# Performance work log

Measured on AMD Instinct MI355X. Metric: run time of the kernel, lower is better.

Reference implementation:

```python
import jax, jax.numpy as jnp
import numpy as np

EPS = 1e-8  # EPS is referenced but undefined in the original source; standard small epsilon


def setup_inputs() -> dict:
    key = jax.random.key(0)
    ks = jax.random.split(key, 12)
    B, T, F = 8, 512, 512
    H, maxlen = 8, 1024
    dh = F // H
    s = 0.02
    return {
        "x": jax.random.normal(ks[0], (B, T, F), jnp.float32),
        "Wq": jax.random.normal(ks[1], (F, F), jnp.float32) * s,
        "bq": jax.random.normal(ks[2], (F,), jnp.float32) * s,
        "Wk": jax.random.normal(ks[3], (F, F), jnp.float32) * s,
        "bk": jax.random.normal(ks[4], (F,), jnp.float32) * s,
        "Wv": jax.random.normal(ks[5], (F, F), jnp.float32) * s,
        "bv": jax.random.normal(ks[6], (F,), jnp.float32) * s,
        "Wo": jax.random.normal(ks[7], (F, F), jnp.float32) * s,
        "bo": jax.random.normal(ks[8], (F,), jnp.float32) * s,
        "delta": jnp.ones((1,), jnp.float32),
        "cache_k": jax.random.normal(ks[9], (B * H, maxlen, dh), jnp.float32),
        "cache_v": jax.random.normal(ks[10], (B * H, maxlen, dh), jnp.float32),
    }


def _to_heads(y, B, T, H, dh):
    # torch.cat(torch.split(y, dh, dim=-1), dim=0): head-major (H*B, T, dh)
    return y.reshape(B, T, H, dh).transpose(2, 0, 1, 3).reshape(H * B, T, dh)


def reference(x, Wq, bq, Wk, bk, Wv, bv, Wo, bo, delta, cache_k, cache_v):
    B, T, F = x.shape
    maxlen, dh = cache_k.shape[1], cache_k.shape[2]
    H = F // dh

    q = _to_heads(x @ Wq.T + bq, B, T, H, dh)  # (HB, T, dh)
    k_new = _to_heads(x @ Wk.T + bk, B, T, H, dh)
    v_new = _to_heads(x @ Wv.T + bv, B, T, H, dh)

    # streaming cache: drop oldest T frames, append new
    k = jnp.concatenate([cache_k[:, T:], k_new], axis=1)  # (HB, maxlen, dh)
    v = jnp.concatenate([cache_v[:, T:], v_new], axis=1)

    # Gaussian relative-position mask G[i,j] = exp(-(i-j)^2 / (delta^2 + EPS))
    ind = jnp.arange(1, maxlen + 1, dtype=x.dtype)
    diff = ind[:, None] - ind[None, :]
    G = jnp.exp(-(diff ** 2) / (delta[0] ** 2 + EPS))  # (maxlen, maxlen)

    d = jnp.sqrt(jnp.asarray(F, jnp.float32)).astype(x.dtype)
    scores = jnp.einsum("btd,bsd->bts", q, k) * G[-T:][None] / d  # (HB, T, maxlen)
    attn = jax.nn.softmax(scores, axis=-1)
    out = jnp.einsum("bts,bsd->btd", attn, v)  # (HB, T, dh)

    # undo head-major split: cat(split(out, B, dim=0), dim=-1)
    out = out.reshape(H, B, T, dh).transpose(1, 2, 0, 3).reshape(B, T, F)
    return out @ Wo.T + bo
```

## Files before the change

### kernel.cpp

```cpp
#include <hip/hip_runtime.h>

typedef __bf16 bf16;
typedef __bf16 bf16x8 __attribute__((ext_vector_type(8)));
typedef __bf16 bf16x4 __attribute__((ext_vector_type(4)));
typedef float f32x4 __attribute__((ext_vector_type(4)));
typedef float f32x16 __attribute__((ext_vector_type(16)));

#define MFMA16(a, b, c) __builtin_amdgcn_mfma_f32_16x16x32_bf16((a), (b), (c), 0, 0, 0)
#define MFMA32(a, b, c) __builtin_amdgcn_mfma_f32_32x32x16_bf16((a), (b), (c), 0, 0, 0)

__device__ __forceinline__ void gload_lds16(const void* g, void* l) {
  __builtin_amdgcn_global_load_lds(
      (const __attribute__((address_space(1))) void*)g,
      (__attribute__((address_space(3))) void*)l, 16, 0, 0);
}

__global__ __launch_bounds__(256) void prep_all(
    const float* __restrict__ x, const float* __restrict__ w0, const float* __restrict__ w1,
    const float* __restrict__ w2, const float* __restrict__ w3, const float* __restrict__ delta,
    const float* __restrict__ ck, const float* __restrict__ cv,
    bf16* __restrict__ xb, bf16* __restrict__ o0, bf16* __restrict__ o1,
    bf16* __restrict__ o2, bf16* __restrict__ o3, float* __restrict__ gt,
    bf16* __restrict__ kk, bf16* __restrict__ vt) {
  const int bid = blockIdx.x;
  const int tid = threadIdx.x;
  __shared__ bf16 tl[64][65];

  if (bid < 2048) {
    const int i = (bid * 256 + tid) * 4;
    f32x4 v = *(const f32x4*)(x + i);
    bf16x4 o;
    o[0] = (bf16)v[0]; o[1] = (bf16)v[1]; o[2] = (bf16)v[2]; o[3] = (bf16)v[3];
    *(bf16x4*)(xb + i) = o;
  } else if (bid < 3072) {
    const int wb = bid - 2048;
    const int widx = wb >> 8;
    const float* s = widx == 0 ? w0 : widx == 1 ? w1 : widx == 2 ? w2 : w3;
    bf16* d = widx == 0 ? o0 : widx == 1 ? o1 : widx == 2 ? o2 : o3;
    const int i = ((wb & 255) * 256 + tid) * 4;
    f32x4 v = *(const f32x4*)(s + i);
    bf16x4 o;
    o[0] = (bf16)v[0]; o[1] = (bf16)v[1]; o[2] = (bf16)v[2]; o[3] = (bf16)v[3];
    *(bf16x4*)(d + i) = o;
  } else if (bid < 3584) {
    const int b2 = bid - 3072;
    const int hb = b2 >> 3;
    const int s0 = (b2 & 7) * 64;
#pragma unroll
    for (int it = 0; it < 16; ++it) {
      int idx = it * 256 + tid;
      int sl = idx >> 6, dd = idx & 63;
      float kval = ck[((size_t)hb * 1024 + 512 + s0 + sl) * 64 + dd];
      kk[((size_t)hb * 1024 + s0 + sl) * 64 + dd] = (bf16)kval;
      float vval = cv[((size_t)hb * 1024 + 512 + s0 + sl) * 64 + dd];
      tl[sl][dd] = (bf16)vval;
    }
    __syncthreads();
#pragma unroll
    for (int it = 0; it < 16; ++it) {
      int idx = it * 256 + tid;
      int dl = idx >> 6, sl = idx & 63;
      vt[((size_t)hb * 64 + dl) * 1024 + s0 + sl] = tl[sl][dl];
    }
  } else {
    const int i = (bid - 3584) * 256 + tid;
    if (i < 1535) {
      float dl = delta[0];
      float inv = 1.0f / (dl * dl + 1e-8f);
      float diff = (float)(i - 511);
      gt[i] = __expf(-diff * diff * inv) * 0.04419417382415922f * 1.4426950408889634f;
    }
  }
}

__global__ __launch_bounds__(256) void qkv_gemm(const bf16* __restrict__ xb,
                                                const bf16* __restrict__ wq, const bf16* __restrict__ wk,
                                                const bf16* __restrict__ wv,
                                                const float* __restrict__ bq, const float* __restrict__ bk,
                                                const float* __restrict__ bv,
                                                bf16* __restrict__ qh, bf16* __restrict__ kk,
                                                bf16* __restrict__ vt) {
  __shared__ bf16 As[128 * 32];
  __shared__ bf16 Bs[64 * 32];
  const int tid = threadIdx.x;
  const int lane = tid & 63;
  const int wave = tid >> 6;
  const int l15 = lane & 15, lg = lane >> 4;
  const int mbase = blockIdx.x * 128;
  const int nfull = blockIdx.y * 64;
  const int mid = nfull >> 9;
  const int nbase = nfull & 511;
  const bf16* W = mid == 0 ? wq : (mid == 1 ? wk : wv);
  const float* bias = mid == 0 ? bq : (mid == 1 ? bk : bv);
  f32x4 acc[2][4] = {};

  const int oB = tid * 16;
  const int rowB = oB >> 6;
  const int cbB = oB & 63;
  for (int k0 = 0; k0 < 512; k0 += 32) {
    __syncthreads();
#pragma unroll
    for (int t = 0; t < 2; ++t) {
      const int oA = (t * 256 + tid) * 16;
      gload_lds16((const char*)(xb + (size_t)(mbase + (oA >> 6)) * 512 + k0) + (oA & 63),
                  (char*)As + oA);
    }
    gload_lds16((const char*)(W + (size_t)(nbase + rowB) * 512 + k0) + cbB, (char*)Bs + oB);
    __syncthreads();
    bf16x8 af[2], bfr[4];
#pragma unroll
    for (int i = 0; i < 2; ++i)
      af[i] = *(const bf16x8*)(As + (wave * 32 + i * 16 + l15) * 32 + lg * 8);
#pragma unroll
    for (int j = 0; j < 4; ++j)
      bfr[j] = *(const bf16x8*)(Bs + (j * 16 + l15) * 32 + lg * 8);
#pragma unroll
    for (int i = 0; i < 2; ++i)
#pragma unroll
      for (int j = 0; j < 4; ++j)
        acc[i][j] = MFMA16(af[i], bfr[j], acc[i][j]);
  }

#pragma unroll
  for (int j = 0; j < 4; ++j) {
    const int nn = nbase + j * 16 + l15;
    const float bvv = bias[nn];
    const int h = nn >> 6, dd = nn & 63;
#pragma unroll
    for (int i = 0; i < 2; ++i) {
#pragma unroll
      for (int r = 0; r < 4; ++r) {
        const int mr = mbase + wave * 32 + i * 16 + lg * 4 + r;
        const float v = acc[i][j][r] + bvv;
        const int bb = mr >> 9, t = mr & 511;
        if (mid == 0) {
          qh[(((size_t)(h * 8 + bb) * 512 + t) << 6) + dd] = (bf16)v;
        } else if (mid == 1) {
          kk[(((size_t)(h * 8 + bb) * 1024 + 512 + t) << 6) + dd] = (bf16)v;
        } else {
          vt[(((size_t)(h * 8 + bb) * 64 + dd) << 10) + 512 + t] = (bf16)v;
        }
      }
    }
  }
}

__global__ __launch_bounds__(256) void out_gemm(const bf16* __restrict__ A,
                                                const bf16* __restrict__ W,
                                                const float* __restrict__ bias,
                                                float* __restrict__ out) {
  __shared__ bf16 As[64 * 32];
  __shared__ bf16 Bs[64 * 32];
  const int tid = threadIdx.x;
  const int lane = tid & 63;
  const int wave = tid >> 6;
  const int wr = wave >> 1, wc = wave & 1;
  const int l15 = lane & 15, lg = lane >> 4;
  const int mbase = blockIdx.x * 64;
  const int nbase = blockIdx.y * 64;
  f32x4 acc[2][2] = {};

  const int o = tid * 16;
  const int row = o >> 6;
  const int cb = o & 63;
  for (int k0 = 0; k0 < 512; k0 += 32) {
    __syncthreads();
    gload_lds16((const char*)(A + (size_t)(mbase + row) * 512 + k0) + cb, (char*)As + o);
    gload_lds16((const char*)(W + (size_t)(nbase + row) * 512 + k0) + cb, (char*)Bs + o);
    __syncthreads();
    bf16x8 af[2], bfr[2];
#pragma unroll
    for (int i = 0; i < 2; ++i)
      af[i] = *(const bf16x8*)(As + (wr * 32 + i * 16 + l15) * 32 + lg * 8);
#pragma unroll
    for (int j = 0; j < 2; ++j)
      bfr[j] = *(const bf16x8*)(Bs + (wc * 32 + j * 16 + l15) * 32 + lg * 8);
#pragma unroll
    for (int i = 0; i < 2; ++i)
#pragma unroll
      for (int j = 0; j < 2; ++j)
        acc[i][j] = MFMA16(af[i], bfr[j], acc[i][j]);
  }

#pragma unroll
  for (int j = 0; j < 2; ++j) {
    const int nn = nbase + wc * 32 + j * 16 + l15;
    const float bvv = bias[nn];
#pragma unroll
    for (int i = 0; i < 2; ++i) {
#pragma unroll
      for (int r = 0; r < 4; ++r) {
        const int mr = mbase + wr * 32 + i * 16 + lg * 4 + r;
        out[(size_t)mr * 512 + nn] = acc[i][j][r] + bvv;
      }
    }
  }
}

__global__ __launch_bounds__(256) void attn_k(const bf16* __restrict__ qh,
                                              const bf16* __restrict__ kk,
                                              const bf16* __restrict__ vt,
                                              const float* __restrict__ gtab,
                                              bf16* __restrict__ ao) {
  const int bid = blockIdx.x;
  const int xcd = bid & 7;
  const int g = bid >> 3;
  const int hb = xcd * 8 + (g >> 3);
  const int qp = g & 7;
  const int tid = threadIdx.x;
  const int lane = tid & 63;
  const int wave = tid >> 6;
  const int l31 = lane & 31;
  const int hi = lane >> 5;
  const int qtile = qp * 2 + (wave & 1);
  const int kvhalf = wave >> 1;
  const int qbase = qtile * 32;
  const int t = qbase + l31;

  __shared__ float gl[1536];
  __shared__ __align__(16) bf16 pbuf[4][32][40];
  __shared__ float mbuf[2][64][33];
  __shared__ float mlb[2][64][2];

  for (int i = tid; i < 1535; i += 256) gl[i] = gtab[i];

  const bf16* qrow = qh + ((size_t)hb * 512 + t) * 64 + hi * 8;
  bf16x8 qf0 = *(const bf16x8*)(qrow);
  bf16x8 qf1 = *(const bf16x8*)(qrow + 16);
  bf16x8 qf2 = *(const bf16x8*)(qrow + 32);
  bf16x8 qf3 = *(const bf16x8*)(qrow + 48);

  const bf16* kbase = kk + (size_t)hb * 1024 * 64;
  const bf16* vbase = vt + (size_t)hb * 64 * 1024;
  const bf16* krow = kbase + (size_t)l31 * 64 + hi * 8;
  const bf16* vrow = vbase + (size_t)l31 * 1024 + hi * 8;

  const int sb0 = kvhalf * 512;
  float m_r = -3.0e38f, l_r = 0.f;
  f32x16 accA = {}, accB = {};

  __syncthreads();

  bf16x8 kc0, kc1, kc2, kc3, kn0, kn1, kn2, kn3;
  {
    const bf16* kp = krow + (size_t)sb0 * 64;
    kc0 = *(const bf16x8*)(kp);
    kc1 = *(const bf16x8*)(kp + 16);
    kc2 = *(const bf16x8*)(kp + 32);
    kc3 = *(const bf16x8*)(kp + 48);
  }

#define ATTN_STEP(C0, C1, C2, C3, N0, N1, N2, N3, SB, PF)                       \
  {                                                                             \
    f32x16 c = {};                                                              \
    c = MFMA32(C0, qf0, c);                                                     \
    c = MFMA32(C1, qf1, c);                                                     \
    c = MFMA32(C2, qf2, c);                                                     \
    c = MFMA32(C3, qf3, c);                                                     \
    if (PF) {                                         \
      const bf16* kp_ = krow + (size_t)((SB) + 32) * 64;                        \
      N0 = *(const bf16x8*)(kp_);                                               \
      N1 = *(const bf16x8*)(kp_ + 16);                                          \
      N2 = *(const bf16x8*)(kp_ + 32);                                          \
      N3 = *(const bf16x8*)(kp_ + 48);                                          \
    }                                                                           \
                                                   \
    const bf16* vp_ = vrow + (SB);                                              \
    bf16x8 vf00 = *(const bf16x8*)(vp_);                                        \
    bf16x8 vf01 = *(const bf16x8*)(vp_ + 16);                                   \
    bf16x8 vf10 = *(const bf16x8*)(vp_ + 32768);                                \
    bf16x8 vf11 = *(const bf16x8*)(vp_ + 32768 + 16);                           \
     \
    const int BASE = 1023 + t - (SB)-4 * hi;                                    \
    float x[16];                                                                \
    _Pragma("unroll") for (int gq = 0; gq < 4; ++gq)                            \
        _Pragma("unroll") for (int j = 0; j < 4; ++j)                           \
            x[gq * 4 + j] = c[gq * 4 + j] * gl[BASE - 8 * gq - j];              \
    float pm = x[0];                                                            \
    _Pragma("unroll") for (int r = 1; r < 16; ++r) pm = fmaxf(pm, x[r]);        \
    pm = fmaxf(pm, __shfl_xor(pm, 32, 64));                                     \
    if (!__all(pm <= m_r + 12.0f)) {             \
      const float mn = fmaxf(m_r, pm);                                          \
      const float fac = exp2f(m_r - mn);                                        \
      m_r = mn;                                                                 \
      l_r *= fac;                                                               \
      _Pragma("unroll") for (int r = 0; r < 16; ++r) {                          \
        accA[r] *= fac;                                                         \
        accB[r] *= fac;                                                         \
      }                                                                         \
    }                                                                           \
    float ps = 0.f;                                                             \
    float e[16];                                                                \
    _Pragma("unroll") for (int r = 0; r < 16; ++r) {                            \
      e[r] = exp2f(x[r] - m_r);                                                 \
      ps += e[r];                                                               \
    }                                                                           \
                      \
    _Pragma("unroll") for (int gq = 0; gq < 4; ++gq) {                          \
      bf16x4 pw;                                                                \
      _Pragma("unroll") for (int j = 0; j < 4; ++j) pw[j] = (bf16)e[gq * 4 + j];\
      *(bf16x4*)&pbuf[wave][l31][4 * hi + 8 * gq] = pw;                         \
    }                                                                           \
    ps += __shfl_xor(ps, 32, 64);                                               \
    l_r += ps;                                                                  \
    asm volatile("s_waitcnt lgkmcnt(0)" ::: "memory");                          \
    __builtin_amdgcn_sched_barrier(0);                                          \
                  \
    bf16x8 P0 = *(const bf16x8*)&pbuf[wave][l31][8 * hi];                       \
    bf16x8 P1 = *(const bf16x8*)&pbuf[wave][l31][16 + 8 * hi];                  \
    accA = MFMA32(vf00, P0, accA);                                              \
    accA = MFMA32(vf01, P1, accA);                                              \
    accB = MFMA32(vf10, P0, accB);                                              \
    accB = MFMA32(vf11, P1, accB);                                              \
  }

  int sb = sb0;
#pragma unroll 1
  for (int it2 = 0; it2 < 8; ++it2) {
    ATTN_STEP(kc0, kc1, kc2, kc3, kn0, kn1, kn2, kn3, sb, true);
    ATTN_STEP(kn0, kn1, kn2, kn3, kc0, kc1, kc2, kc3, sb + 32, it2 < 7);
    sb += 64;
  }
#undef ATTN_STEP

  __syncthreads();
  const int slot = wave & 1;
  if (kvhalf == 1) {
#pragma unroll
    for (int r = 0; r < 16; ++r) {
      mbuf[slot][lane][r] = accA[r];
      mbuf[slot][lane][16 + r] = accB[r];
    }
    mlb[slot][lane][0] = m_r;
    mlb[slot][lane][1] = l_r;
  }
  __syncthreads();
  if (kvhalf == 0) {
    const float mp = mlb[slot][lane][0];
    const float lp = mlb[slot][lane][1];
    const float M = fmaxf(m_r, mp);
    const float f0 = exp2f(m_r - M);
    const float f1 = exp2f(mp - M);
    const float linv = 1.0f / (l_r * f0 + lp * f1);
    const int b = hb & 7, h = hb >> 3;
    bf16* obase = ao + ((size_t)(b * 512 + t) * 512) + h * 64;
#pragma unroll
    for (int D = 0; D < 2; ++D) {
#pragma unroll
      for (int gq = 0; gq < 4; ++gq) {
        bf16x4 ov;
#pragma unroll
        for (int j = 0; j < 4; ++j) {
          const float own = D ? accB[gq * 4 + j] : accA[gq * 4 + j];
          const float oth = mbuf[slot][lane][D * 16 + gq * 4 + j];
          ov[j] = (bf16)((own * f0 + oth * f1) * linv);
        }
        *(bf16x4*)(obase + D * 32 + gq * 8 + hi * 4) = ov;
      }
    }
  }
}

extern "C" void kernel_launch(void* const* d_in, const int* in_sizes, int n_in,
                              void* d_out, int out_size, void* d_ws, size_t ws_size,
                              hipStream_t stream) {
  const float* x = (const float*)d_in[0];
  const float* Wq = (const float*)d_in[1];
  const float* bq = (const float*)d_in[2];
  const float* Wk = (const float*)d_in[3];
  const float* bk = (const float*)d_in[4];
  const float* Wv = (const float*)d_in[5];
  const float* bv = (const float*)d_in[6];
  const float* Wo = (const float*)d_in[7];
  const float* bo = (const float*)d_in[8];
  const float* delta = (const float*)d_in[9];
  const float* ck = (const float*)d_in[10];
  const float* cv = (const float*)d_in[11];

  char* w = (char*)d_ws;
  auto carve = [&](size_t bytes) {
    char* p = w;
    w += (bytes + 255) & ~(size_t)255;
    return p;
  };
  bf16* xb = (bf16*)carve((size_t)4096 * 512 * 2);
  bf16* wqb = (bf16*)carve((size_t)512 * 512 * 2);
  bf16* wkb = (bf16*)carve((size_t)512 * 512 * 2);
  bf16* wvb = (bf16*)carve((size_t)512 * 512 * 2);
  bf16* wob = (bf16*)carve((size_t)512 * 512 * 2);
  bf16* qhb = (bf16*)carve((size_t)64 * 512 * 64 * 2);
  bf16* kkb = (bf16*)carve((size_t)64 * 1024 * 64 * 2);
  bf16* vtb = (bf16*)carve((size_t)64 * 64 * 1024 * 2);
  bf16* aob = (bf16*)carve((size_t)4096 * 512 * 2);
  float* gt = (float*)carve(1536 * 4);

  prep_all<<<3590, 256, 0, stream>>>(x, Wq, Wk, Wv, Wo, delta, ck, cv,
                                     xb, wqb, wkb, wvb, wob, gt, kkb, vtb);
  qkv_gemm<<<dim3(32, 24), 256, 0, stream>>>(xb, wqb, wkb, wvb, bq, bk, bv, qhb, kkb, vtb);
  attn_k<<<512, 256, 0, stream>>>(qhb, kkb, vtb, gt, aob);
  out_gemm<<<dim3(64, 8), 256, 0, stream>>>(aob, wob, bo, (float*)d_out);
}
```

Before: 71.64 us.

## Split attention KV range four ways per block with one query tile

Each attention block now processes a single 32-row query tile, with its four waves each covering a quarter of the 1024 keys, and the grid doubles to 1024 blocks. Wave 0 merges the partial softmax states of the other three waves through shared memory, which is now a union reused between the P buffer and the merge buffers. The aim is more parallelism and shorter per-wave loops. In exchange, Q fragments and the Gaussian table are loaded twice as often and the final merge is longer.

```diff
diff --git a/kernel.cpp b/kernel.cpp
--- a/kernel.cpp
+++ b/kernel.cpp
@@ -205,22 +205,21 @@
   const int bid = blockIdx.x;
   const int xcd = bid & 7;
   const int g = bid >> 3;
-  const int hb = xcd * 8 + (g >> 3);
-  const int qp = g & 7;
+  const int hb = xcd * 8 + (g >> 4);
+  const int qtile = g & 15;
   const int tid = threadIdx.x;
   const int lane = tid & 63;
   const int wave = tid >> 6;
   const int l31 = lane & 31;
   const int hi = lane >> 5;
-  const int qtile = qp * 2 + (wave & 1);
-  const int kvhalf = wave >> 1;
   const int qbase = qtile * 32;
   const int t = qbase + l31;
 
   __shared__ float gl[1536];
-  __shared__ __align__(16) bf16 pbuf[4][32][40];
-  __shared__ float mbuf[2][64][33];
-  __shared__ float mlb[2][64][2];
+  __shared__ __align__(16) char un[26880];
+  bf16 (*pbuf)[32][40] = (bf16(*)[32][40])un;
+  float (*mbuf)[64][33] = (float(*)[64][33])un;
+  float (*mlb)[64][2] = (float(*)[64][2])(un + 25344);
 
   for (int i = tid; i < 1535; i += 256) gl[i] = gtab[i];
 
@@ -235,7 +234,7 @@
   const bf16* krow = kbase + (size_t)l31 * 64 + hi * 8;
   const bf16* vrow = vbase + (size_t)l31 * 1024 + hi * 8;
 
-  const int sb0 = kvhalf * 512;
+  const int sb0 = wave * 256;
   float m_r = -3.0e38f, l_r = 0.f;
   f32x16 accA = {}, accB = {};
 
@@ -270,7 +269,7 @@
     bf16x8 vf01 = *(const bf16x8*)(vp_ + 16);                                   \
     bf16x8 vf10 = *(const bf16x8*)(vp_ + 32768);                                \
     bf16x8 vf11 = *(const bf16x8*)(vp_ + 32768 + 16);                           \
-     \
+                 \
     const int BASE = 1023 + t - (SB)-4 * hi;                                    \
     float x[16];                                                                \
     _Pragma("unroll") for (int gq = 0; gq < 4; ++gq)                            \
@@ -316,16 +315,16 @@
 
   int sb = sb0;
 #pragma unroll 1
-  for (int it2 = 0; it2 < 8; ++it2) {
+  for (int it2 = 0; it2 < 4; ++it2) {
     ATTN_STEP(kc0, kc1, kc2, kc3, kn0, kn1, kn2, kn3, sb, true);
-    ATTN_STEP(kn0, kn1, kn2, kn3, kc0, kc1, kc2, kc3, sb + 32, it2 < 7);
+    ATTN_STEP(kn0, kn1, kn2, kn3, kc0, kc1, kc2, kc3, sb + 32, it2 < 3);
     sb += 64;
   }
 #undef ATTN_STEP
 
   __syncthreads();
-  const int slot = wave & 1;
-  if (kvhalf == 1) {
+  if (wave > 0) {
+    const int slot = wave - 1;
 #pragma unroll
     for (int r = 0; r < 16; ++r) {
       mbuf[slot][lane][r] = accA[r];
@@ -335,13 +334,23 @@
     mlb[slot][lane][1] = l_r;
   }
   __syncthreads();
-  if (kvhalf == 0) {
-    const float mp = mlb[slot][lane][0];
-    const float lp = mlb[slot][lane][1];
-    const float M = fmaxf(m_r, mp);
-    const float f0 = exp2f(m_r - M);
-    const float f1 = exp2f(mp - M);
-    const float linv = 1.0f / (l_r * f0 + lp * f1);
+  if (wave == 0) {
+#pragma unroll
+    for (int p = 0; p < 3; ++p) {
+      const float mp = mlb[p][lane][0];
+      const float lp = mlb[p][lane][1];
+      const float M = fmaxf(m_r, mp);
+      const float f0 = exp2f(m_r - M);
+      const float f1 = exp2f(mp - M);
+      l_r = l_r * f0 + lp * f1;
+      m_r = M;
+#pragma unroll
+      for (int r = 0; r < 16; ++r) {
+        accA[r] = accA[r] * f0 + mbuf[p][lane][r] * f1;
+        accB[r] = accB[r] * f0 + mbuf[p][lane][16 + r] * f1;
+      }
+    }
+    const float linv = 1.0f / l_r;
     const int b = hb & 7, h = hb >> 3;
     bf16* obase = ao + ((size_t)(b * 512 + t) * 512) + h * 64;
 #pragma unroll
@@ -352,8 +361,7 @@
 #pragma unroll
         for (int j = 0; j < 4; ++j) {
           const float own = D ? accB[gq * 4 + j] : accA[gq * 4 + j];
-          const float oth = mbuf[slot][lane][D * 16 + gq * 4 + j];
-          ov[j] = (bf16)((own * f0 + oth * f1) * linv);
+          ov[j] = (bf16)(own * linv);
         }
         *(bf16x4*)(obase + D * 32 + gq * 8 + hi * 4) = ov;
       }
@@ -397,6 +405,6 @@
   prep_all<<<3590, 256, 0, stream>>>(x, Wq, Wk, Wv, Wo, delta, ck, cv,
                                      xb, wqb, wkb, wvb, wob, gt, kkb, vtb);
   qkv_gemm<<<dim3(32, 24), 256, 0, stream>>>(xb, wqb, wkb, wvb, bq, bk, bv, qhb, kkb, vtb);
-  attn_k<<<512, 256, 0, stream>>>(qhb, kkb, vtb, gt, aob);
+  attn_k<<<1024, 256, 0, stream>>>(qhb, kkb, vtb, gt, aob);
   out_gemm<<<dim3(64, 8), 256, 0, stream>>>(aob, wob, bo, (float*)d_out);
 }
```

Measured after the change: 73.27 us. +2.3%, slower.
